# Kernel optimization log

Measured on AMD Instinct MI355X. Metric: run time of the kernel, lower is better.

The kernel has to match this reference:

```python
import jax, jax.numpy as jnp
import numpy as np

OUT, IN = 8192, 8192
TOKENS = 32


def setup_inputs() -> dict:
    key = jax.random.key(0)
    k_in, k_w, k_zp, k_s, k_b = jax.random.split(key, 5)
    return {
        "input": jax.random.normal(k_in, (TOKENS, IN), dtype=jnp.float32),
        # int8 quantized weight stored as the compressed parameter
        "weight_packed": jax.random.randint(k_w, (OUT, IN), -128, 128, dtype=jnp.int32).astype(jnp.int8),
        # per-output-channel asymmetric zero point and scale
        "weight_zero_point": jax.random.randint(k_zp, (OUT, 1), -8, 8, dtype=jnp.int32).astype(jnp.int8),
        "weight_scale": (jax.random.uniform(k_s, (OUT, 1), dtype=jnp.float32) * 0.01 + 1e-4),
        "bias": jax.random.normal(k_b, (OUT,), dtype=jnp.float32),
    }


def reference(input, weight_packed, weight_zero_point, weight_scale, bias):
    # Compressor.decompress_module: dequantize int8 weight per output channel
    # w[o, i] = (q[o, i] - zp[o]) * scale[o]   -> fp32 [OUT, IN]
    w = (weight_packed.astype(jnp.int32) - weight_zero_point.astype(jnp.int32)).astype(jnp.float32) * weight_scale
    # F.linear(input, w, bias): [T, IN] @ [OUT, IN]^T + [OUT]
    return jnp.einsum("ti,oi->to", input, w) + bias
```

## Files before the change

kernel.cpp:

```cpp
#include <hip/hip_runtime.h>
#include <stdint.h>

#define TOKENS 32
#define IN_DIM 8192
#define OUT_DIM 8192
#define NWAVE 2
#define BK 128
#define KRANGE (IN_DIM / NWAVE)
#define NCHUNK (KRANGE / BK)

typedef __bf16 bf16x8 __attribute__((ext_vector_type(8)));
typedef float f32x16 __attribute__((ext_vector_type(16)));

static __device__ __forceinline__ uint32_t pk_bf16_2(float f0, float f1) {
    return __builtin_amdgcn_perm(__float_as_uint(f1), __float_as_uint(f0), 0x07060302u);
}
static __device__ __forceinline__ float trunc_bf(float f) {
    return __uint_as_float(__float_as_uint(f) & 0xffff0000u);
}

__global__ __launch_bounds__(128, 1) void gemm_kernel(
        const float* __restrict__ in,
        const int* __restrict__ w,
        const int* __restrict__ zp,
        const float* __restrict__ scale,
        const float* __restrict__ bias,
        float* __restrict__ out) {
    __shared__ int lds[NWAVE][2][32][BK];

    const int tid   = threadIdx.x;
    const int wv    = tid >> 6;
    const int lane  = tid & 63;
    const int lo    = lane & 31;
    const int hi    = lane >> 5;
    const int obase = blockIdx.x * 32;
    const int k0    = wv * KRANGE;

    const int l5 = lane & 31;
    const int r0 = hi;

    auto stage = [&](int c, int b) {
#pragma unroll
        for (int p = 0; p < 16; ++p) {
            const int r  = p * 2 + r0;
            const int swr = (r & 7) << 2;
            const int* g = w + (size_t)(obase + r) * IN_DIM + k0 + c * BK
                             + ((l5 * 4) ^ swr);
            __builtin_amdgcn_global_load_lds(
                (const __attribute__((address_space(1))) void*)g,
                (__attribute__((address_space(3))) void*)&lds[wv][b][p * 2][0],
                16, 0, 0);
        }
    };

    const float* ain = in + (size_t)lo * IN_DIM + k0 + hi * 8;
    auto aload = [&](int c, float4 (&ab)[16]) {
#pragma unroll
        for (int j = 0; j < 16; ++j)
            ab[j] = *reinterpret_cast<const float4*>(ain + c * BK + (j >> 1) * 16 + (j & 1) * 4);
    };

    f32x16 acc;
#pragma unroll
    for (int i = 0; i < 16; ++i) acc[i] = 0.f;
    float rs = 0.f;

    const int sw = (lo & 7) << 2;
    const int* lrow0 = &lds[wv][0][lo][0];
    const int* lrow1 = &lds[wv][1][lo][0];

    auto compute = [&](const int* lrow, const float4 (&ab)[16]) {
#pragma unroll
        for (int s = 0; s < 8; ++s) {
            const int d0 = s * 16 + hi * 8;
            const float4 a0 = ab[2 * s];
            const float4 a1 = ab[2 * s + 1];
            int4 b0 = *reinterpret_cast<const int4*>(lrow + (d0 ^ sw));
            int4 b1 = *reinterpret_cast<const int4*>(lrow + ((d0 + 4) ^ sw));

            rs += trunc_bf(a0.x) + trunc_bf(a0.y) + trunc_bf(a0.z) + trunc_bf(a0.w)
                + trunc_bf(a1.x) + trunc_bf(a1.y) + trunc_bf(a1.z) + trunc_bf(a1.w);

            union { uint32_t u[4]; bf16x8 v; } af, bf_;
            af.u[0] = pk_bf16_2(a0.x, a0.y);
            af.u[1] = pk_bf16_2(a0.z, a0.w);
            af.u[2] = pk_bf16_2(a1.x, a1.y);
            af.u[3] = pk_bf16_2(a1.z, a1.w);
            bf_.u[0] = pk_bf16_2((float)b0.x, (float)b0.y);
            bf_.u[1] = pk_bf16_2((float)b0.z, (float)b0.w);
            bf_.u[2] = pk_bf16_2((float)b1.x, (float)b1.y);
            bf_.u[3] = pk_bf16_2((float)b1.z, (float)b1.w);

            acc = __builtin_amdgcn_mfma_f32_32x32x16_bf16(af.v, bf_.v, acc, 0, 0, 0);
        }
    };

    float4 ab0[16], ab1[16];

    stage(0, 0);
    aload(0, ab0);
    for (int cc = 0; cc < NCHUNK; cc += 2) {
        stage(cc + 1, 1);
        aload(cc + 1, ab1);
        asm volatile("s_waitcnt vmcnt(32)" ::: "memory");
        compute(lrow0, ab0);

        if (cc + 2 < NCHUNK) {
            stage(cc + 2, 0);
            aload(cc + 2, ab0);
            asm volatile("s_waitcnt vmcnt(32)" ::: "memory");
        } else {
            asm volatile("s_waitcnt vmcnt(0)" ::: "memory");
        }
        compute(lrow1, ab1);
    }

    rs += __shfl_down(rs, 32);
    __syncthreads();
    float* red = (float*)&lds[0][0][0][0];
    float* rsl = red + NWAVE * TOKENS * 32;
#pragma unroll
    for (int r = 0; r < 16; ++r) {
        const int m = (r & 3) + 8 * (r >> 2) + 4 * hi;
        red[wv * (TOKENS * 32) + m * 32 + lo] = acc[r];
    }
    if (lane < 32) rsl[wv * 32 + lane] = rs;
    __syncthreads();

    for (int idx = tid; idx < TOKENS * 32; idx += 128) {
        const int m = idx >> 5;
        const int o = obase + (idx & 31);
        float s    = red[idx] + red[TOKENS * 32 + idx];
        float rsum = rsl[m] + rsl[32 + m];
        out[(size_t)m * OUT_DIM + o] = scale[o] * (s - (float)zp[o] * rsum) + bias[o];
    }
}

extern "C" void kernel_launch(void* const* d_in, const int* in_sizes, int n_in,
                              void* d_out, int out_size, void* d_ws, size_t ws_size,
                              hipStream_t stream) {
    const float* in    = (const float*)d_in[0];
    const int*   wq    = (const int*)d_in[1];
    const int*   zp    = (const int*)d_in[2];
    const float* scale = (const float*)d_in[3];
    const float* bias  = (const float*)d_in[4];
    float* out = (float*)d_out;

    gemm_kernel<<<OUT_DIM / 32, 128, 0, stream>>>(in, wq, zp, scale, bias, out);
}
```

Baseline: 369.0 us.

## Split K across slabs and pre-convert activations to bf16 in a prep kernel

Adds a prep kernel that converts the activations to bf16 once and computes the per-token row sums. The GEMM then splits K into 4 slabs, launching four times as many blocks, and writes partial tiles to workspace. A reduce kernel sums the partials and applies the zero-point, scale and bias epilogue. This aims to raise occupancy from 256 blocks and remove redundant per-block activation conversion, at the cost of two extra launches and partial-sum traffic.

Result: no change. 366.3 us (-0.7%).

```diff
diff --git a/kernel.cpp b/kernel.cpp
--- a/kernel.cpp
+++ b/kernel.cpp
@@ -4,10 +4,13 @@
 #define TOKENS 32
 #define IN_DIM 8192
 #define OUT_DIM 8192
+#define SLABS 4
+#define KSLAB (IN_DIM / SLABS)
 #define NWAVE 2
+#define KRANGE (KSLAB / NWAVE)
 #define BK 128
-#define KRANGE (IN_DIM / NWAVE)
 #define NCHUNK (KRANGE / BK)
+#define NTILE (OUT_DIM / 32)
 
 typedef __bf16 bf16x8 __attribute__((ext_vector_type(8)));
 typedef float f32x16 __attribute__((ext_vector_type(16)));
@@ -19,13 +22,38 @@
     return __uint_as_float(__float_as_uint(f) & 0xffff0000u);
 }
 
+__global__ __launch_bounds__(256) void prep_kernel(const float* __restrict__ in,
+                                                   uint16_t* __restrict__ abf,
+                                                   float* __restrict__ rowsum) {
+    const int t = blockIdx.x;
+    const int tid = threadIdx.x;
+    const float4* __restrict__ row = reinterpret_cast<const float4*>(in + (size_t)t * IN_DIM);
+    ushort4* __restrict__ orow = reinterpret_cast<ushort4*>(abf + (size_t)t * IN_DIM);
+    float s = 0.f;
+#pragma unroll
+    for (int it = 0; it < IN_DIM / 4 / 256; ++it) {
+        const int i4 = it * 256 + tid;
+        float4 v = row[i4];
+        s += trunc_bf(v.x) + trunc_bf(v.y) + trunc_bf(v.z) + trunc_bf(v.w);
+        ushort4 b;
+        b.x = (uint16_t)(__float_as_uint(v.x) >> 16);
+        b.y = (uint16_t)(__float_as_uint(v.y) >> 16);
+        b.z = (uint16_t)(__float_as_uint(v.z) >> 16);
+        b.w = (uint16_t)(__float_as_uint(v.w) >> 16);
+        orow[i4] = b;
+    }
+#pragma unroll
+    for (int off = 32; off > 0; off >>= 1) s += __shfl_down(s, off);
+    __shared__ float wred[4];
+    if ((tid & 63) == 0) wred[tid >> 6] = s;
+    __syncthreads();
+    if (tid == 0) rowsum[t] = wred[0] + wred[1] + wred[2] + wred[3];
+}
+
 __global__ __launch_bounds__(128, 1) void gemm_kernel(
-        const float* __restrict__ in,
+        const uint16_t* __restrict__ abf,
         const int* __restrict__ w,
-        const int* __restrict__ zp,
-        const float* __restrict__ scale,
-        const float* __restrict__ bias,
-        float* __restrict__ out) {
+        float* __restrict__ parts) {
     __shared__ int lds[NWAVE][2][32][BK];
 
     const int tid   = threadIdx.x;
@@ -33,19 +61,18 @@
     const int lane  = tid & 63;
     const int lo    = lane & 31;
     const int hi    = lane >> 5;
-    const int obase = blockIdx.x * 32;
-    const int k0    = wv * KRANGE;
-
-    const int l5 = lane & 31;
-    const int r0 = hi;
+    const int slab  = blockIdx.x & (SLABS - 1);
+    const int tile  = blockIdx.x >> 2;
+    const int obase = tile * 32;
+    const int k0    = slab * KSLAB + wv * KRANGE;
 
     auto stage = [&](int c, int b) {
 #pragma unroll
         for (int p = 0; p < 16; ++p) {
-            const int r  = p * 2 + r0;
+            const int r   = p * 2 + hi;
             const int swr = (r & 7) << 2;
             const int* g = w + (size_t)(obase + r) * IN_DIM + k0 + c * BK
-                             + ((l5 * 4) ^ swr);
+                             + (((lane & 31) * 4) ^ swr);
             __builtin_amdgcn_global_load_lds(
                 (const __attribute__((address_space(1))) void*)g,
                 (__attribute__((address_space(3))) void*)&lds[wv][b][p * 2][0],
@@ -53,87 +80,102 @@
         }
     };
 
-    const float* ain = in + (size_t)lo * IN_DIM + k0 + hi * 8;
-    auto aload = [&](int c, float4 (&ab)[16]) {
+    const uint16_t* ain = abf + (size_t)lo * IN_DIM + k0 + hi * 8;
+    auto aload = [&](int c, uint4 (&ab)[8]) {
 #pragma unroll
-        for (int j = 0; j < 16; ++j)
-            ab[j] = *reinterpret_cast<const float4*>(ain + c * BK + (j >> 1) * 16 + (j & 1) * 4);
+        for (int s = 0; s < 8; ++s)
+            ab[s] = *reinterpret_cast<const uint4*>(ain + c * BK + s * 16);
     };
 
     f32x16 acc;
 #pragma unroll
     for (int i = 0; i < 16; ++i) acc[i] = 0.f;
-    float rs = 0.f;
 
     const int sw = (lo & 7) << 2;
     const int* lrow0 = &lds[wv][0][lo][0];
     const int* lrow1 = &lds[wv][1][lo][0];
 
-    auto compute = [&](const int* lrow, const float4 (&ab)[16]) {
+    auto compute = [&](const int* lrow, const uint4 (&ab)[8]) {
 #pragma unroll
         for (int s = 0; s < 8; ++s) {
             const int d0 = s * 16 + hi * 8;
-            const float4 a0 = ab[2 * s];
-            const float4 a1 = ab[2 * s + 1];
             int4 b0 = *reinterpret_cast<const int4*>(lrow + (d0 ^ sw));
             int4 b1 = *reinterpret_cast<const int4*>(lrow + ((d0 + 4) ^ sw));
-
-            rs += trunc_bf(a0.x) + trunc_bf(a0.y) + trunc_bf(a0.z) + trunc_bf(a0.w)
-                + trunc_bf(a1.x) + trunc_bf(a1.y) + trunc_bf(a1.z) + trunc_bf(a1.w);
-
-            union { uint32_t u[4]; bf16x8 v; } af, bf_;
-            af.u[0] = pk_bf16_2(a0.x, a0.y);
-            af.u[1] = pk_bf16_2(a0.z, a0.w);
-            af.u[2] = pk_bf16_2(a1.x, a1.y);
-            af.u[3] = pk_bf16_2(a1.z, a1.w);
+            union { uint4 u; bf16x8 v; } af;
+            af.u = ab[s];
+            union { uint32_t u[4]; bf16x8 v; } bf_;
             bf_.u[0] = pk_bf16_2((float)b0.x, (float)b0.y);
             bf_.u[1] = pk_bf16_2((float)b0.z, (float)b0.w);
             bf_.u[2] = pk_bf16_2((float)b1.x, (float)b1.y);
             bf_.u[3] = pk_bf16_2((float)b1.z, (float)b1.w);
-
             acc = __builtin_amdgcn_mfma_f32_32x32x16_bf16(af.v, bf_.v, acc, 0, 0, 0);
         }
     };
 
-    float4 ab0[16], ab1[16];
+    uint4 ab0[8], ab1[8];
 
     stage(0, 0);
     aload(0, ab0);
     for (int cc = 0; cc < NCHUNK; cc += 2) {
         stage(cc + 1, 1);
         aload(cc + 1, ab1);
-        asm volatile("s_waitcnt vmcnt(32)" ::: "memory");
+        asm volatile("s_waitcnt vmcnt(24)" ::: "memory");
         compute(lrow0, ab0);
 
         if (cc + 2 < NCHUNK) {
             stage(cc + 2, 0);
             aload(cc + 2, ab0);
-            asm volatile("s_waitcnt vmcnt(32)" ::: "memory");
+            asm volatile("s_waitcnt vmcnt(24)" ::: "memory");
         } else {
             asm volatile("s_waitcnt vmcnt(0)" ::: "memory");
         }
         compute(lrow1, ab1);
     }
 
-    rs += __shfl_down(rs, 32);
     __syncthreads();
     float* red = (float*)&lds[0][0][0][0];
-    float* rsl = red + NWAVE * TOKENS * 32;
 #pragma unroll
     for (int r = 0; r < 16; ++r) {
         const int m = (r & 3) + 8 * (r >> 2) + 4 * hi;
         red[wv * (TOKENS * 32) + m * 32 + lo] = acc[r];
     }
-    if (lane < 32) rsl[wv * 32 + lane] = rs;
     __syncthreads();
 
-    for (int idx = tid; idx < TOKENS * 32; idx += 128) {
-        const int m = idx >> 5;
-        const int o = obase + (idx & 31);
-        float s    = red[idx] + red[TOKENS * 32 + idx];
-        float rsum = rsl[m] + rsl[32 + m];
-        out[(size_t)m * OUT_DIM + o] = scale[o] * (s - (float)zp[o] * rsum) + bias[o];
+    float* pt = parts + (size_t)(slab * NTILE + tile) * (TOKENS * 32);
+    for (int idx = tid; idx < TOKENS * 32; idx += 128)
+        pt[idx] = red[idx] + red[TOKENS * 32 + idx];
+}
+
+__global__ __launch_bounds__(256) void reduce_kernel(
+        const float* __restrict__ parts,
+        const float* __restrict__ rowsum,
+        const int* __restrict__ zp,
+        const float* __restrict__ scale,
+        const float* __restrict__ bias,
+        float* __restrict__ out) {
+    const int tile = blockIdx.x;
+    const int idx  = threadIdx.x * 4;
+    const int m    = idx >> 5;
+    const int n    = idx & 31;
+    const int o    = tile * 32 + n;
+
+    float4 s = make_float4(0.f, 0.f, 0.f, 0.f);
+#pragma unroll
+    for (int sl = 0; sl < SLABS; ++sl) {
+        float4 p = *reinterpret_cast<const float4*>(
+            parts + (size_t)(sl * NTILE + tile) * (TOKENS * 32) + idx);
+        s.x += p.x; s.y += p.y; s.z += p.z; s.w += p.w;
     }
+    const float rs = rowsum[m];
+    const float4 sc = *reinterpret_cast<const float4*>(scale + o);
+    const float4 bi = *reinterpret_cast<const float4*>(bias + o);
+    const int4   zv = *reinterpret_cast<const int4*>(zp + o);
+    float4 r;
+    r.x = sc.x * (s.x - (float)zv.x * rs) + bi.x;
+    r.y = sc.y * (s.y - (float)zv.y * rs) + bi.y;
+    r.z = sc.z * (s.z - (float)zv.z * rs) + bi.z;
+    r.w = sc.w * (s.w - (float)zv.w * rs) + bi.w;
+    *reinterpret_cast<float4*>(out + (size_t)m * OUT_DIM + o) = r;
 }
 
 extern "C" void kernel_launch(void* const* d_in, const int* in_sizes, int n_in,
@@ -146,5 +188,11 @@
     const float* bias  = (const float*)d_in[4];
     float* out = (float*)d_out;
 
-    gemm_kernel<<<OUT_DIM / 32, 128, 0, stream>>>(in, wq, zp, scale, bias, out);
+    uint16_t* abf    = (uint16_t*)d_ws;
+    float*    rowsum = (float*)((char*)d_ws + (512u << 10));
+    float*    parts  = (float*)((char*)d_ws + (1u << 20));
+
+    prep_kernel<<<TOKENS, 256, 0, stream>>>(in, abf, rowsum);
+    gemm_kernel<<<SLABS * NTILE, 128, 0, stream>>>(abf, wq, parts);
+    reduce_kernel<<<NTILE, 256, 0, stream>>>(parts, rowsum, zp, scale, bias, out);
 }
```
